# Kernel tuning notes

Hardware: AMD Instinct MI355X
Metric: run time of the kernel (lower is better)

## Reference

```python
import jax, jax.numpy as jnp
import numpy as np

S, K, O = 8192, 1024, 4096  # seq_len, in_features, out_features


def setup_inputs() -> dict:
    key = jax.random.key(0)
    k1, k2, k3, k4, k5 = jax.random.split(key, 5)
    x = jax.random.randint(k1, (S, K), -128, 128, dtype=jnp.int8)
    weight_q = jax.random.randint(k2, (O, K), -128, 128, dtype=jnp.int8)
    scale_x = jax.random.uniform(k3, (), jnp.float32, 0.01, 0.1)
    scale_w = jax.random.uniform(k4, (), jnp.float32, 0.01, 0.1)
    scale_y = jax.random.uniform(k5, (S,), jnp.float32, 0.5, 2.0)  # per-row output scale
    return {"x": x, "weight_q": weight_q, "scale_x": scale_x,
            "scale_w": scale_w, "scale_y": scale_y}


def reference(x, weight_q, scale_x, scale_w, scale_y):
    # int8 GEMM with int32 accumulation: [S,K] @ [O,K]^T -> [S,O]
    acc = jnp.einsum('sk,ok->so', x.astype(jnp.int32), weight_q.astype(jnp.int32))
    # fused per-row requantization: scale_y[:seq_len] gives per-row scale
    requant_scale = (scale_x * scale_w / scale_y).astype(jnp.float32)  # [S]
    scaled = acc.astype(jnp.float32) * requant_scale[:, None]
    out_q = jnp.clip(jnp.round(scaled), -128.0, 127.0).astype(jnp.int8)
    return out_q, scale_y
```

## Files before the change

### kernel.cpp

```cpp
#include <hip/hip_runtime.h>


#define S_DIM 8192
#define K_DIM 1024
#define O_DIM 4096
#define BM 256
#define BN 256
#define BK 64
#define NITER (K_DIM / BK)
#define TILE_BYTES (128 * BK)
#define BAND_BYTES (NITER * TILE_BYTES)
#define A_SLOT (2 * TILE_BYTES)
#define B_SLOT (2 * TILE_BYTES)

using i32x4 = __attribute__((ext_vector_type(4))) int;

__device__ __forceinline__ void load_lds16(const void* g, void* l) {
  __builtin_amdgcn_global_load_lds(
      (const __attribute__((address_space(1))) void*)g,
      (__attribute__((address_space(3))) void*)l, 16, 0, 0);
}

#define FENCE() asm volatile("" ::: "memory")
#define BARRIER() asm volatile("s_barrier" ::: "memory")

__global__ void pack_kernel(const int* __restrict__ xi, const int* __restrict__ wi,
                            const float* __restrict__ sy,
                            uint4* __restrict__ ap, uint4* __restrict__ bp,
                            float* __restrict__ out_sy) {
  const int tid = blockIdx.x * blockDim.x + threadIdx.x;
  const int nA = S_DIM * K_DIM / 16;
  const int nB = O_DIM * K_DIM / 16;

  const int* src;
  uint4* dst;
  int j;
  if (tid < nA) {
    src = xi; dst = ap; j = tid;
  } else if (tid < nA + nB) {
    src = wi; dst = bp; j = tid - nA;
  } else {
    return;
  }
  const int t = j >> 9;
  const int idx = j & 511;
  const int r = idx >> 2;
  const int cs = idx & 3;
  const int c = cs ^ (r & 3);
  const int band = t >> 4;
  const int kt = t & 15;
  const int row = band * 128 + r;
  const int4* s4 = (const int4*)src + row * 256 + kt * 16 + c * 4;
  int4 v0 = s4[0], v1 = s4[1], v2 = s4[2], v3 = s4[3];
  uint4 o;
  o.x = (v0.x & 0xff) | ((v0.y & 0xff) << 8) | ((v0.z & 0xff) << 16) | (((unsigned)v0.w & 0xff) << 24);
  o.y = (v1.x & 0xff) | ((v1.y & 0xff) << 8) | ((v1.z & 0xff) << 16) | (((unsigned)v1.w & 0xff) << 24);
  o.z = (v2.x & 0xff) | ((v2.y & 0xff) << 8) | ((v2.z & 0xff) << 16) | (((unsigned)v2.w & 0xff) << 24);
  o.w = (v3.x & 0xff) | ((v3.y & 0xff) << 8) | ((v3.z & 0xff) << 16) | (((unsigned)v3.w & 0xff) << 24);
  dst[j] = o;
  if (tid < S_DIM) out_sy[tid] = sy[tid];
}

__global__ __launch_bounds__(512, 2) void gemm_i8_kernel(
    const signed char* __restrict__ Ap,
    const signed char* __restrict__ Bp,
    const float* __restrict__ sx, const float* __restrict__ sw,
    const float* __restrict__ sy, float* __restrict__ out) {
  __shared__ __align__(16) signed char As[3][A_SLOT];
  __shared__ __align__(16) signed char Bs[3][B_SLOT];

  const int tid = threadIdx.x;
  const int wave = tid >> 6;
  const int lane = tid & 63;
  const int wm = wave >> 2;
  const int wn = wave & 3;
  const int rowBase = blockIdx.x * BM;
  const int colBase = blockIdx.y * BN;

  const int soff = wave * 1024 + lane * 16;
  const signed char* gA0 = Ap + (size_t)(2 * blockIdx.x) * BAND_BYTES + soff;
  const signed char* gA1 = Ap + (size_t)(2 * blockIdx.x + 1) * BAND_BYTES + soff;
  const signed char* gB0 = Bp + (size_t)(2 * blockIdx.y) * BAND_BYTES + soff;
  const signed char* gB1 = Bp + (size_t)(2 * blockIdx.y + 1) * BAND_BYTES + soff;
  signed char* ldsA = (signed char*)As + soff;
  signed char* ldsB = (signed char*)Bs + soff;

  i32x4 acc[8][4] = {};

  const int fr = lane & 15;
  const int fq = (((lane >> 4) ^ (fr & 3)) & 3) * 16;

  const int aoff = wm * TILE_BYTES + fr * 64 + fq;
  const int boff = (wn >> 1) * TILE_BYTES + ((wn & 1) * 64 + fr) * 64 + fq;

  load_lds16(gA0, ldsA);
  load_lds16(gA1, ldsA + TILE_BYTES);
  load_lds16(gB0, ldsB);
  load_lds16(gB1, ldsB + TILE_BYTES);
  FENCE();
  load_lds16(gA0 + TILE_BYTES, ldsA + A_SLOT);
  load_lds16(gA1 + TILE_BYTES, ldsA + A_SLOT + TILE_BYTES);
  load_lds16(gB0 + TILE_BYTES, ldsB + B_SLOT);
  load_lds16(gB1 + TILE_BYTES, ldsB + B_SLOT + TILE_BYTES);

#pragma unroll
  for (int it = 0; it < NITER; ++it) {
    if (it + 1 < NITER) {
      asm volatile("s_waitcnt vmcnt(4) lgkmcnt(0)" ::: "memory");
    } else {
      asm volatile("s_waitcnt vmcnt(0) lgkmcnt(0)" ::: "memory");
    }
    BARRIER();

    const signed char* curA = As[it % 3] + aoff;
    const signed char* curB = Bs[it % 3] + boff;
    const int pslot = (it + 2) % 3;
    const size_t pgoff = (size_t)(it + 2) * TILE_BYTES;
    const bool pf = (it + 2) < NITER;

    i32x4 bf[4];
#pragma unroll
    for (int p = 0; p < 4; ++p) {
      if (p == 0) {
#pragma unroll
        for (int ni = 0; ni < 4; ++ni)
          bf[ni] = *(const i32x4*)(curB + ni * 1024);
      }
      i32x4 af0 = *(const i32x4*)(curA + (2 * p) * 1024);
      i32x4 af1 = *(const i32x4*)(curA + (2 * p + 1) * 1024);

      if (pf) {
        if (p == 0) load_lds16(gA0 + pgoff, ldsA + pslot * A_SLOT);
        if (p == 1) load_lds16(gA1 + pgoff, ldsA + pslot * A_SLOT + TILE_BYTES);
        if (p == 2) load_lds16(gB0 + pgoff, ldsB + pslot * B_SLOT);
        if (p == 3) load_lds16(gB1 + pgoff, ldsB + pslot * B_SLOT + TILE_BYTES);
      }

      BARRIER();
      __builtin_amdgcn_s_setprio(1);
#pragma unroll
      for (int ni = 0; ni < 4; ++ni) {
        acc[2 * p][ni] =
            __builtin_amdgcn_mfma_i32_16x16x64_i8(af0, bf[ni], acc[2 * p][ni], 0, 0, 0);
        acc[2 * p + 1][ni] =
            __builtin_amdgcn_mfma_i32_16x16x64_i8(af1, bf[ni], acc[2 * p + 1][ni], 0, 0, 0);
      }
      __builtin_amdgcn_s_setprio(0);
      BARRIER();
    }
  }

  const float sxw = sx[0] * sw[0];
  const int quad = lane >> 4;
#pragma unroll
  for (int mi = 0; mi < 8; ++mi) {
#pragma unroll
    for (int r = 0; r < 4; ++r) {
      const int s = rowBase + wm * 128 + mi * 16 + quad * 4 + r;
      const float rs = sxw / sy[s];
      float* orow = out + (size_t)s * O_DIM + colBase + wn * 64 + fr;
#pragma unroll
      for (int ni = 0; ni < 4; ++ni) {
        float f = rintf((float)acc[mi][ni][r] * rs);
        f = fminf(127.0f, fmaxf(-128.0f, f));
        orow[ni * 16] = f;
      }
    }
  }
}

extern "C" void kernel_launch(void* const* d_in, const int* in_sizes, int n_in,
                              void* d_out, int out_size, void* d_ws, size_t ws_size,
                              hipStream_t stream) {
  const int* x = (const int*)d_in[0];
  const int* w = (const int*)d_in[1];
  const float* sx = (const float*)d_in[2];
  const float* sw = (const float*)d_in[3];
  const float* sy = (const float*)d_in[4];
  float* out = (float*)d_out;

  uint4* ap = (uint4*)d_ws;
  uint4* bp = ap + (size_t)S_DIM * K_DIM / 16;

  const int total = S_DIM * K_DIM / 16 + O_DIM * K_DIM / 16;
  pack_kernel<<<(total + 255) / 256, 256, 0, stream>>>(
      x, w, sy, ap, bp, out + (size_t)S_DIM * O_DIM);

  dim3 grid(S_DIM / BM, O_DIM / BN);
  gemm_i8_kernel<<<grid, 512, 0, stream>>>(
      (const signed char*)ap, (const signed char*)bp, sx, sw, sy, out);
}
```

Baseline: 212.3 us.

## Deepen LDS pipeline to four stages and halve barriers per K-step

Raises LDS buffering from three to four slots so global-to-LDS prefetch runs three tiles ahead. The inner loop goes from four phases per K tile, each with two barriers, to two larger phases of 16 MFMAs each, with the vmcnt wait moved to the end of the iteration. The aim is to hide more global memory latency and cut barrier overhead. The cost is higher LDS use (128KB per block, since each slot is 16KB), which may limit occupancy under the two-blocks-per-CU launch bound. It also drops the lgkmcnt wait, which leaves the correctness of the LDS read ordering to compiler-inserted waits.

```diff
diff --git a/kernel.cpp b/kernel.cpp
--- a/kernel.cpp
+++ b/kernel.cpp
@@ -22,7 +22,6 @@
 }
 
 #define FENCE() asm volatile("" ::: "memory")
-#define BARRIER() asm volatile("s_barrier" ::: "memory")
 
 __global__ void pack_kernel(const int* __restrict__ xi, const int* __restrict__ wi,
                             const float* __restrict__ sy,
@@ -66,8 +65,8 @@
     const signed char* __restrict__ Bp,
     const float* __restrict__ sx, const float* __restrict__ sw,
     const float* __restrict__ sy, float* __restrict__ out) {
-  __shared__ __align__(16) signed char As[3][A_SLOT];
-  __shared__ __align__(16) signed char Bs[3][B_SLOT];
+  __shared__ __align__(16) signed char As[4][A_SLOT];
+  __shared__ __align__(16) signed char Bs[4][B_SLOT];
 
   const int tid = threadIdx.x;
   const int wave = tid >> 6;
@@ -102,52 +101,71 @@
   load_lds16(gA1 + TILE_BYTES, ldsA + A_SLOT + TILE_BYTES);
   load_lds16(gB0 + TILE_BYTES, ldsB + B_SLOT);
   load_lds16(gB1 + TILE_BYTES, ldsB + B_SLOT + TILE_BYTES);
+  FENCE();
+  load_lds16(gA0 + 2 * TILE_BYTES, ldsA + 2 * A_SLOT);
+  load_lds16(gA1 + 2 * TILE_BYTES, ldsA + 2 * A_SLOT + TILE_BYTES);
+  load_lds16(gB0 + 2 * TILE_BYTES, ldsB + 2 * B_SLOT);
+  load_lds16(gB1 + 2 * TILE_BYTES, ldsB + 2 * B_SLOT + TILE_BYTES);
+  FENCE();
+  asm volatile("s_waitcnt vmcnt(8)" ::: "memory");
+  __builtin_amdgcn_s_barrier();
 
 #pragma unroll
   for (int it = 0; it < NITER; ++it) {
-    if (it + 1 < NITER) {
-      asm volatile("s_waitcnt vmcnt(4) lgkmcnt(0)" ::: "memory");
-    } else {
-      asm volatile("s_waitcnt vmcnt(0) lgkmcnt(0)" ::: "memory");
-    }
-    BARRIER();
-
-    const signed char* curA = As[it % 3] + aoff;
-    const signed char* curB = Bs[it % 3] + boff;
-    const int pslot = (it + 2) % 3;
-    const size_t pgoff = (size_t)(it + 2) * TILE_BYTES;
-    const bool pf = (it + 2) < NITER;
+    const signed char* curA = As[it & 3] + aoff;
+    const signed char* curB = Bs[it & 3] + boff;
+    const int pslot = (it + 3) & 3;
+    const size_t pgoff = (size_t)(it + 3) * TILE_BYTES;
+    const bool pf = (it + 3) < NITER;
 
     i32x4 bf[4];
 #pragma unroll
-    for (int p = 0; p < 4; ++p) {
-      if (p == 0) {
-#pragma unroll
-        for (int ni = 0; ni < 4; ++ni)
-          bf[ni] = *(const i32x4*)(curB + ni * 1024);
-      }
-      i32x4 af0 = *(const i32x4*)(curA + (2 * p) * 1024);
-      i32x4 af1 = *(const i32x4*)(curA + (2 * p + 1) * 1024);
-
-      if (pf) {
-        if (p == 0) load_lds16(gA0 + pgoff, ldsA + pslot * A_SLOT);
-        if (p == 1) load_lds16(gA1 + pgoff, ldsA + pslot * A_SLOT + TILE_BYTES);
-        if (p == 2) load_lds16(gB0 + pgoff, ldsB + pslot * B_SLOT);
-        if (p == 3) load_lds16(gB1 + pgoff, ldsB + pslot * B_SLOT + TILE_BYTES);
-      }
-
-      BARRIER();
-      __builtin_amdgcn_s_setprio(1);
-#pragma unroll
-      for (int ni = 0; ni < 4; ++ni) {
-        acc[2 * p][ni] =
-            __builtin_amdgcn_mfma_i32_16x16x64_i8(af0, bf[ni], acc[2 * p][ni], 0, 0, 0);
-        acc[2 * p + 1][ni] =
-            __builtin_amdgcn_mfma_i32_16x16x64_i8(af1, bf[ni], acc[2 * p + 1][ni], 0, 0, 0);
-      }
-      __builtin_amdgcn_s_setprio(0);
-      BARRIER();
-    }
+    for (int ni = 0; ni < 4; ++ni)
+      bf[ni] = *(const i32x4*)(curB + ni * 1024);
+    i32x4 af[4];
+#pragma unroll
+    for (int mi = 0; mi < 4; ++mi)
+      af[mi] = *(const i32x4*)(curA + mi * 1024);
+    if (pf) {
+      load_lds16(gA0 + pgoff, ldsA + pslot * A_SLOT);
+      load_lds16(gA1 + pgoff, ldsA + pslot * A_SLOT + TILE_BYTES);
+    }
+    __builtin_amdgcn_s_barrier();
+    __builtin_amdgcn_s_setprio(1);
+#pragma unroll
+    for (int mi = 0; mi < 4; ++mi)
+#pragma unroll
+      for (int ni = 0; ni < 4; ++ni)
+        acc[mi][ni] =
+            __builtin_amdgcn_mfma_i32_16x16x64_i8(af[mi], bf[ni], acc[mi][ni], 0, 0, 0);
+    __builtin_amdgcn_s_setprio(0);
+    __builtin_amdgcn_s_barrier();
+
+#pragma unroll
+    for (int mi = 0; mi < 4; ++mi)
+      af[mi] = *(const i32x4*)(curA + (mi + 4) * 1024);
+    if (pf) {
+      load_lds16(gB0 + pgoff, ldsB + pslot * B_SLOT);
+      load_lds16(gB1 + pgoff, ldsB + pslot * B_SLOT + TILE_BYTES);
+    }
+    __builtin_amdgcn_s_barrier();
+    __builtin_amdgcn_s_setprio(1);
+#pragma unroll
+    for (int mi = 0; mi < 4; ++mi)
+#pragma unroll
+      for (int ni = 0; ni < 4; ++ni)
+        acc[mi + 4][ni] =
+            __builtin_amdgcn_mfma_i32_16x16x64_i8(af[mi], bf[ni], acc[mi + 4][ni], 0, 0, 0);
+    __builtin_amdgcn_s_setprio(0);
+
+    if (it + 3 < NITER) {
+      asm volatile("s_waitcnt vmcnt(8)" ::: "memory");
+    } else if (it + 2 < NITER) {
+      asm volatile("s_waitcnt vmcnt(4)" ::: "memory");
+    } else if (it + 1 < NITER) {
+      asm volatile("s_waitcnt vmcnt(0)" ::: "memory");
+    }
+    __builtin_amdgcn_s_barrier();
   }
 
   const float sxw = sx[0] * sw[0];
```

Result: no change. 209.0 us (-1.6%).
